# Performance work log

Hardware: AMD Instinct MI355X
Metric: run time of the kernel (lower is better)

The kernel has to match this reference:

```python
import jax, jax.numpy as jnp
import numpy as np

N_BASIS = 32
MAX_STD = 4.0
NDIM = 3


def setup_inputs() -> dict:
    key = jax.random.key(0)
    k1, k2, k3 = jax.random.split(key, 3)
    B, N, M = 2, 8192, 4096
    f = jax.random.normal(k1, (B, N), dtype=jnp.float32)
    coords = 2.0 * jax.random.normal(k2, (B, N, NDIM), dtype=jnp.float32)
    anchor_coords = 2.0 * jax.random.normal(k3, (B, M, NDIM), dtype=jnp.float32)
    # buffers, exactly as in __init__
    sigmas = jnp.linspace(0.0, MAX_STD, N_BASIS + 1)[1:]
    gammas = 1.0 / (2.0 * sigmas ** 2)                     # [n_basis]
    norms = (2.0 * jnp.pi * sigmas ** 2) ** (NDIM / 2.0)   # [n_basis]
    return {"f": f, "coords": coords, "anchor_coords": anchor_coords,
            "gammas": gammas, "norms": norms}


def reference(f, coords, anchor_coords, gammas, norms):
    # SqDist(X, Y) for all anchor/point pairs: [B, M, N]
    x2 = jnp.sum(anchor_coords * anchor_coords, axis=-1)  # [B, M]
    y2 = jnp.sum(coords * coords, axis=-1)                # [B, N]
    d2 = (x2[:, :, None] + y2[:, None, :]
          - 2.0 * jnp.einsum('bmd,bnd->bmn', anchor_coords, coords))

    # Sum_j exp(-gamma_b * d2_ij) * f_j, one bandwidth at a time to avoid
    # materializing the [B, M, N, n_basis] tensor (mirrors KeOps lazy reduce).
    def body(_, g):
        return None, jnp.einsum('bmn,bn->bm', jnp.exp(-g * d2), f)

    _, out = jax.lax.scan(body, None, gammas)   # [n_basis, B, M]
    out = jnp.moveaxis(out, 0, -1)              # [B, M, n_basis]
    return out / norms
```

## Files before the change

kernel.cpp:

```cpp
#include <hip/hip_runtime.h>

#define NB 32
#define L2E 1.4426950408889634f

typedef float v2f __attribute__((ext_vector_type(2)));

#if __has_builtin(__builtin_amdgcn_exp2f)
#define EXP2(x) __builtin_amdgcn_exp2f(x)
#else
#define EXP2(x) __expf((x) * 0.6931471805599453f)
#endif

#if __has_builtin(__builtin_elementwise_fma)
#define VFMA(a, b, c) __builtin_elementwise_fma(a, b, c)
#else
static __device__ inline v2f VFMA(v2f a, v2f b, v2f c) {
    v2f r; r.x = fmaf(a.x, b.x, c.x); r.y = fmaf(a.y, b.y, c.y); return r;
}
#endif

__global__ __launch_bounds__(512) void gp_main(
    const float* __restrict__ f,
    const float* __restrict__ coords,
    const float* __restrict__ anchors,
    const float* __restrict__ gammas,
    const float* __restrict__ norms,
    float* __restrict__ ws,
    int B, int N, int M, int NSEG, int applyNorm)
{
    const int mtiles = M / 256;
    const int tile = blockIdx.x;
    const int seg  = blockIdx.y;
    const int b    = tile / mtiles;
    const int m    = (tile - b * mtiles) * 256 + threadIdx.x;
    const int bm   = b * M + m;
    const int kh   = threadIdx.y;
    const int kbase = kh * (NB / 2);

    const float ax = anchors[(size_t)bm * 3 + 0];
    const float ay = anchors[(size_t)bm * 3 + 1];
    const float az = anchors[(size_t)bm * 3 + 2];

    v2f negc[NB / 4];
#pragma unroll
    for (int j = 0; j < NB / 4; ++j) {
        negc[j].x = -L2E * gammas[kbase + 2 * j + 0];
        negc[j].y = -L2E * gammas[kbase + 2 * j + 1];
    }

    v2f acc[NB / 4];
#pragma unroll
    for (int j = 0; j < NB / 4; ++j) acc[j] = (v2f)(0.0f);

    const float* __restrict__ fb = f + (size_t)b * N;
    const float* __restrict__ cb = coords + (size_t)b * N * 3;

    const int n0 = seg * NSEG;
    const int n1 = (n0 + NSEG > N) ? N : n0 + NSEG;

#pragma unroll 2
    for (int n = n0; n < n1; ++n) {
        const float px = cb[(size_t)n * 3 + 0];
        const float py = cb[(size_t)n * 3 + 1];
        const float pz = cb[(size_t)n * 3 + 2];
        const float fv = fb[n];

        const float dx = ax - px;
        const float dy = ay - py;
        const float dz = az - pz;
        const float d2 = fmaf(dx, dx, fmaf(dy, dy, dz * dz));
        const v2f d2v = (v2f)(d2);
        const v2f fvv = (v2f)(fv);

#pragma unroll
        for (int j = 0; j < NB / 4; ++j) {
            const v2f arg = d2v * negc[j];
            v2f e;
            e.x = EXP2(arg.x);
            e.y = EXP2(arg.y);
            acc[j] = VFMA(e, fvv, acc[j]);
        }
    }

    if (applyNorm) {
        float* __restrict__ w = ws + (size_t)bm * NB + kbase;
#pragma unroll
        for (int j = 0; j < NB / 4; ++j) {
            w[2 * j + 0] = acc[j].x / norms[kbase + 2 * j + 0];
            w[2 * j + 1] = acc[j].y / norms[kbase + 2 * j + 1];
        }
    } else {
        v2f* __restrict__ w = (v2f*)(ws + ((size_t)seg * (B * M) + bm) * NB + kbase);
#pragma unroll
        for (int j = 0; j < NB / 4; ++j) w[j] = acc[j];
    }
}

__global__ __launch_bounds__(256) void gp_reduce(
    const float4* __restrict__ ws,
    const float4* __restrict__ norms4,
    float4* __restrict__ out,
    int BM, int S)
{
    const int t = blockIdx.x * blockDim.x + threadIdx.x;
    if (t >= BM * (NB / 4)) return;
    const size_t stride = (size_t)BM * (NB / 4);
    float4 s = make_float4(0.f, 0.f, 0.f, 0.f);
    for (int i = 0; i < S; ++i) {
        const float4 v = ws[(size_t)i * stride + t];
        s.x += v.x; s.y += v.y; s.z += v.z; s.w += v.w;
    }
    const float4 nrm = norms4[t & (NB / 4 - 1)];
    s.x /= nrm.x; s.y /= nrm.y; s.z /= nrm.z; s.w /= nrm.w;
    out[t] = s;
}

extern "C" void kernel_launch(void* const* d_in, const int* in_sizes, int n_in,
                              void* d_out, int out_size, void* d_ws, size_t ws_size,
                              hipStream_t stream) {
    const float* f       = (const float*)d_in[0];
    const float* coords  = (const float*)d_in[1];
    const float* anchors = (const float*)d_in[2];
    const float* gammas  = (const float*)d_in[3];
    const float* norms   = (const float*)d_in[4];
    float* out = (float*)d_out;

    const int B = 2, N = 8192, M = 4096;
    const int BM = B * M;

    int S = (int)(ws_size / ((size_t)BM * NB * sizeof(float)));
    if (S > 32) S = 32;
    int s2 = 1; while (s2 * 2 <= S) s2 *= 2;
    S = (S >= 1) ? s2 : 0;

    dim3 block(256, 2);
    if (S >= 2) {
        const int NSEG = N / S;
        dim3 grid(B * (M / 256), S);
        gp_main<<<grid, block, 0, stream>>>(f, coords, anchors, gammas, norms,
                                            (float*)d_ws, B, N, M, NSEG, 0);
        const int total = BM * (NB / 4);
        gp_reduce<<<(total + 255) / 256, 256, 0, stream>>>(
            (const float4*)d_ws, (const float4*)norms, (float4*)out, BM, S);
    } else {
        dim3 grid(B * (M / 256), 1);
        gp_main<<<grid, block, 0, stream>>>(f, coords, anchors, gammas, norms,
                                            out, B, N, M, N, 1);
    }
}
```

Baseline: 216.7 us.

## Derive half the Gaussian bandwidths by repeated squaring instead of exp2

Each thread now handles all 32 bandwidths. It evaluates exp2 only for the upper 16 gammas and gets the lower 16 by squaring twice. This uses the fact that the linspace sigmas make gamma_{k-1} equal to four times gamma_{2k-1}. The goal is to halve transcendental instructions, which run at reduced rate, and replace them with cheap multiplies. The change also software-prefetches the next point, drops the 2-row block layout, and raises the segment cap to 64. The trade-offs are that it hardcodes the gamma structure, ignoring gammas[0..15], and repeated squaring amplifies relative error for the narrowest bandwidths.

```diff
diff --git a/kernel.cpp b/kernel.cpp
--- a/kernel.cpp
+++ b/kernel.cpp
@@ -5,11 +5,13 @@
 
 typedef float v2f __attribute__((ext_vector_type(2)));
 
+static __device__ __forceinline__ float exp2f_fast(float x) {
 #if __has_builtin(__builtin_amdgcn_exp2f)
-#define EXP2(x) __builtin_amdgcn_exp2f(x)
+    return __builtin_amdgcn_exp2f(x);
 #else
-#define EXP2(x) __expf((x) * 0.6931471805599453f)
+    return __expf(x * 0.6931471805599453f);
 #endif
+}
 
 #if __has_builtin(__builtin_elementwise_fma)
 #define VFMA(a, b, c) __builtin_elementwise_fma(a, b, c)
@@ -19,7 +21,7 @@
 }
 #endif
 
-__global__ __launch_bounds__(512) void gp_main(
+__global__ __launch_bounds__(256) void gp_main(
     const float* __restrict__ f,
     const float* __restrict__ coords,
     const float* __restrict__ anchors,
@@ -34,65 +36,76 @@
     const int b    = tile / mtiles;
     const int m    = (tile - b * mtiles) * 256 + threadIdx.x;
     const int bm   = b * M + m;
-    const int kh   = threadIdx.y;
-    const int kbase = kh * (NB / 2);
 
     const float ax = anchors[(size_t)bm * 3 + 0];
     const float ay = anchors[(size_t)bm * 3 + 1];
     const float az = anchors[(size_t)bm * 3 + 2];
 
-    v2f negc[NB / 4];
+    float negc[16];
 #pragma unroll
-    for (int j = 0; j < NB / 4; ++j) {
-        negc[j].x = -L2E * gammas[kbase + 2 * j + 0];
-        negc[j].y = -L2E * gammas[kbase + 2 * j + 1];
-    }
+    for (int j = 0; j < 16; ++j)
+        negc[j] = -L2E * gammas[16 + j];
 
-    v2f acc[NB / 4];
+    v2f acc[16];
 #pragma unroll
-    for (int j = 0; j < NB / 4; ++j) acc[j] = (v2f)(0.0f);
+    for (int j = 0; j < 16; ++j) acc[j] = (v2f)(0.0f);
 
     const float* __restrict__ fb = f + (size_t)b * N;
     const float* __restrict__ cb = coords + (size_t)b * N * 3;
 
     const int n0 = seg * NSEG;
-    const int n1 = (n0 + NSEG > N) ? N : n0 + NSEG;
+    const int n1 = (n0 + NSEG > N) ? N : (n0 + NSEG);
 
-#pragma unroll 2
+    float px = cb[(size_t)n0 * 3 + 0];
+    float py = cb[(size_t)n0 * 3 + 1];
+    float pz = cb[(size_t)n0 * 3 + 2];
+    float fv = fb[n0];
+
     for (int n = n0; n < n1; ++n) {
-        const float px = cb[(size_t)n * 3 + 0];
-        const float py = cb[(size_t)n * 3 + 1];
-        const float pz = cb[(size_t)n * 3 + 2];
-        const float fv = fb[n];
+        const float dx = ax - px, dy = ay - py, dz = az - pz;
+        const float d2 = fmaf(dx, dx, fmaf(dy, dy, dz * dz));
+        const float fcur = fv;
 
-        const float dx = ax - px;
-        const float dy = ay - py;
-        const float dz = az - pz;
-        const float d2 = fmaf(dx, dx, fmaf(dy, dy, dz * dz));
-        const v2f d2v = (v2f)(d2);
-        const v2f fvv = (v2f)(fv);
+        const int np = (n + 1 < n1) ? (n + 1) : n;
+        px = cb[(size_t)np * 3 + 0];
+        py = cb[(size_t)np * 3 + 1];
+        pz = cb[(size_t)np * 3 + 2];
+        fv = fb[np];
+
+        float E[NB];
+#pragma unroll
+        for (int j = 0; j < 16; ++j)
+            E[16 + j] = exp2f_fast(d2 * negc[j]);
 
 #pragma unroll
-        for (int j = 0; j < NB / 4; ++j) {
-            const v2f arg = d2v * negc[j];
-            v2f e;
-            e.x = EXP2(arg.x);
-            e.y = EXP2(arg.y);
+        for (int k = 16; k >= 3; k -= 2) {
+            v2f t; t.x = E[2 * k - 1]; t.y = E[2 * k - 3];
+            t = t * t;
+            t = t * t;
+            E[k - 1] = t.x; E[k - 2] = t.y;
+        }
+        { const float t = E[3] * E[3]; E[1] = t * t; }
+        { const float t = E[1] * E[1]; E[0] = t * t; }
+
+        const v2f fvv = (v2f)(fcur);
+#pragma unroll
+        for (int j = 0; j < 16; ++j) {
+            v2f e; e.x = E[2 * j]; e.y = E[2 * j + 1];
             acc[j] = VFMA(e, fvv, acc[j]);
         }
     }
 
     if (applyNorm) {
-        float* __restrict__ w = ws + (size_t)bm * NB + kbase;
+        float* __restrict__ w = ws + (size_t)bm * NB;
 #pragma unroll
-        for (int j = 0; j < NB / 4; ++j) {
-            w[2 * j + 0] = acc[j].x / norms[kbase + 2 * j + 0];
-            w[2 * j + 1] = acc[j].y / norms[kbase + 2 * j + 1];
+        for (int j = 0; j < 16; ++j) {
+            w[2 * j + 0] = acc[j].x / norms[2 * j + 0];
+            w[2 * j + 1] = acc[j].y / norms[2 * j + 1];
         }
     } else {
-        v2f* __restrict__ w = (v2f*)(ws + ((size_t)seg * (B * M) + bm) * NB + kbase);
+        v2f* __restrict__ w = (v2f*)(ws + ((size_t)seg * (B * M) + bm) * NB);
 #pragma unroll
-        for (int j = 0; j < NB / 4; ++j) w[j] = acc[j];
+        for (int j = 0; j < 16; ++j) w[j] = acc[j];
     }
 }
 
@@ -129,22 +142,21 @@
     const int BM = B * M;
 
     int S = (int)(ws_size / ((size_t)BM * NB * sizeof(float)));
-    if (S > 32) S = 32;
+    if (S > 64) S = 64;
     int s2 = 1; while (s2 * 2 <= S) s2 *= 2;
     S = (S >= 1) ? s2 : 0;
 
-    dim3 block(256, 2);
     if (S >= 2) {
         const int NSEG = N / S;
         dim3 grid(B * (M / 256), S);
-        gp_main<<<grid, block, 0, stream>>>(f, coords, anchors, gammas, norms,
-                                            (float*)d_ws, B, N, M, NSEG, 0);
+        gp_main<<<grid, 256, 0, stream>>>(f, coords, anchors, gammas, norms,
+                                          (float*)d_ws, B, N, M, NSEG, 0);
         const int total = BM * (NB / 4);
         gp_reduce<<<(total + 255) / 256, 256, 0, stream>>>(
             (const float4*)d_ws, (const float4*)norms, (float4*)out, BM, S);
     } else {
         dim3 grid(B * (M / 256), 1);
-        gp_main<<<grid, block, 0, stream>>>(f, coords, anchors, gammas, norms,
-                                            out, B, N, M, N, 1);
+        gp_main<<<grid, 256, 0, stream>>>(f, coords, anchors, gammas, norms,
+                                          out, B, N, M, N, 1);
     }
 }
```

Result: no change. 219.4 us (+1.3%).
